# Kernel tuning notes

Measured on AMD Instinct MI355X. Metric: run time of the kernel, lower is better.

## Reference

```python
import math
from itertools import product
import jax, jax.numpy as jnp
import numpy as np

# ---- static config (mirrors LPD.__init__) ----
IMG_W, IMG_H = 1920, 1080
MIN_SIZES = [[10, 16, 24], [32, 48], [64, 96], [128, 192, 256]]
STEPS = [8, 16, 32, 64]
VARIANCE = (0.1, 0.2)
CONF_THR = 0.3
NMS_THR = 0.3
TOP_K = 2000
KEEP_TOP_K = 750
BATCH = 16


def make_priors() -> np.ndarray:
    """Anchor grid in normalized (cx, cy, w, h), kornia _PriorBox order:
    per level, per cell (row-major), per min_size."""
    levels = []
    for step, mss in zip(STEPS, MIN_SIZES):
        fh, fw = math.ceil(IMG_H / step), math.ceil(IMG_W / step)
        ii, jj = np.meshgrid(np.arange(fh), np.arange(fw), indexing='ij')
        cx = (jj + 0.5) * step / IMG_W  # [fh, fw]
        cy = (ii + 0.5) * step / IMG_H
        nms_ = len(mss)
        cx = np.broadcast_to(cx[..., None], (fh, fw, nms_))
        cy = np.broadcast_to(cy[..., None], (fh, fw, nms_))
        skx = np.broadcast_to(np.array(mss, np.float64) / IMG_W, (fh, fw, nms_))
        sky = np.broadcast_to(np.array(mss, np.float64) / IMG_H, (fh, fw, nms_))
        levels.append(np.stack([cx, cy, skx, sky], -1).reshape(-1, 4))
    return np.concatenate(levels, 0).astype(np.float32)  # [N, 4]

N_PRIORS = make_priors().shape[0]  # 119130 for 1920x1080


def decode(loc, priors):
    """loc [B,N,14], priors [N,4] -> scaled [B,N,14] (x1y1x2y2 + 5 landmarks)."""
    var = jnp.asarray(VARIANCE, loc.dtype)
    p_xy, p_wh = priors[:, :2], priors[:, 2:4]
    cxcy = p_xy + loc[..., 0:2] * VARIANCE[0] * p_wh
    wh = p_wh * jnp.exp(loc[..., 2:4] * var)
    x1y1 = cxcy - wh * 0.5
    x2y2 = x1y1 + wh
    # 5 landmark points
    lmk = p_xy[None, :, None, :] + loc[..., 4:14].reshape(*loc.shape[:-1], 5, 2) * VARIANCE[0] * p_wh[None, :, None, :]
    boxes = jnp.concatenate([x1y1, x2y2, lmk.reshape(*loc.shape[:-1], 10)], -1)
    scale = jnp.tile(jnp.asarray([IMG_W, IMG_H], loc.dtype), 7)
    return boxes * scale


def nms_keep(b, s):
    """Greedy NMS. b [K,4] sorted by descending score s [K]. Returns bool keep [K]."""
    area = jnp.clip(b[:, 2] - b[:, 0], 0.0) * jnp.clip(b[:, 3] - b[:, 1], 0.0)
    lt = jnp.maximum(b[:, None, :2], b[None, :, :2])
    rb = jnp.minimum(b[:, None, 2:4], b[None, :, 2:4])
    whi = jnp.clip(rb - lt, 0.0)
    inter = whi[..., 0] * whi[..., 1]
    iou_m = inter / (area[:, None] + area[None, :] - inter + 1e-9)  # [K,K]
    K = b.shape[0]
    idx = jnp.arange(K)

    def step(active, i):
        keep_i = active[i]
        active = active & ~(keep_i & (iou_m[i] > NMS_THR) & (idx > i))
        return active, keep_i

    _, keep = jax.lax.scan(step, s > 0.0, idx)
    return keep


def setup_inputs() -> dict:
    key = jax.random.key(0)
    k1, k2, k3 = jax.random.split(key, 3)
    return {
        'loc': jax.random.normal(k1, (BATCH, N_PRIORS, 14), jnp.float32),
        'conf': jax.random.normal(k2, (BATCH, N_PRIORS, 2), jnp.float32),
        'iou': jax.random.normal(k3, (BATCH, N_PRIORS, 1), jnp.float32),
    }


def reference(loc, conf, iou):
    priors = jnp.asarray(make_priors())  # [N,4] constant
    cls = jax.nn.softmax(conf, axis=-1)[..., 1]          # [B,N]
    iou_s = jnp.clip(iou[..., 0], 0.0, 1.0)
    scores = jnp.sqrt(cls * iou_s)
    scores = jnp.where(scores >= CONF_THR, scores, 0.0)  # confidence threshold
    boxes = decode(loc, priors)                          # [B,N,14]
    top_s, top_i = jax.lax.top_k(scores, TOP_K)          # sorted desc
    boxes_k = jnp.take_along_axis(boxes, top_i[..., None], axis=1)  # [B,K,14]
    keep = jax.vmap(nms_keep)(boxes_k[..., :4], top_s)   # [B,K] bool
    keep = keep & (jnp.cumsum(keep.astype(jnp.int32), axis=-1) <= KEEP_TOP_K)
    dets = jnp.concatenate([boxes_k, (top_s * keep)[..., None]], -1)  # [B,K,15]
    return dets
```

## Files before the change

### kernel.cpp

```cpp
#include <hip/hip_runtime.h>
#include <math.h>

#define BB 16
#define TOPK 2000
#define KEEPK 750
#define CAND_CAP 4096
#define EDGE_CAP 8192
#define HIST_BINS 256
#define BIN_BASE 0x3E99u

__global__ __launch_bounds__(256) void k_scores(const float* __restrict__ conf,
                                                const float* __restrict__ iou,
                                                unsigned* __restrict__ sbits,
                                                unsigned* __restrict__ hist,
                                                unsigned* __restrict__ ccount,
                                                unsigned* __restrict__ ecount,
                                                unsigned* __restrict__ tdone,
                                                int N, int nchunk) {
  __shared__ unsigned h[HIST_BINS];
  int b = blockIdx.y;
  int tid = threadIdx.x;
  for (int i = tid; i < HIST_BINS; i += 256) h[i] = 0;
  if (blockIdx.x == 0) {
    if (tid == 0) ccount[b] = 0;
    if (tid == 1) ecount[b] = 0;
    if (tid == 2) tdone[b] = 0;
  }
  __syncthreads();
  const float2* c2 = (const float2*)conf + (size_t)b * N;
  const float* iu = iou + (size_t)b * N;
  unsigned* sb = sbits + (size_t)b * N;
  int n0 = blockIdx.x * 4096;
#pragma unroll 4
  for (int k = 0; k < 16; ++k) {
    int n = n0 + k * 256 + tid;
    if (n < N) {
      float2 c = c2[n];
      float m = fmaxf(c.x, c.y);
      float e0 = (float)exp((double)(c.x - m));
      float e1 = (float)exp((double)(c.y - m));
      float p1 = e1 / (e0 + e1);
      float ic = fminf(fmaxf(iu[n], 0.0f), 1.0f);
      float s = sqrtf(p1 * ic);
      s = (s >= 0.3f) ? s : 0.0f;
      unsigned bits = __float_as_uint(s);
      sb[n] = bits;
      if (bits != 0u) {
        int bin = (int)(bits >> 16) - (int)BIN_BASE;
        bin = bin < 0 ? 0 : (bin > 255 ? 255 : bin);
        atomicAdd(&h[bin], 1u);
      }
    }
  }
  __syncthreads();
  unsigned* hdst = hist + ((size_t)b * nchunk + blockIdx.x) * HIST_BINS;
  for (int i = tid; i < HIST_BINS; i += 256) hdst[i] = h[i];
}

__global__ __launch_bounds__(256) void k_compact(const unsigned* __restrict__ sbits,
                                                 const unsigned* __restrict__ hist,
                                                 unsigned* __restrict__ ccount,
                                                 unsigned long long* __restrict__ ckeys,
                                                 int N, int nchunk) {
  __shared__ unsigned sT;
  __shared__ unsigned long long masks[32];
  __shared__ unsigned wioff[32];
  __shared__ unsigned blockbase;
  int b = blockIdx.y;
  int tid = threadIdx.x, lane = tid & 63, wv = tid >> 6;

  if (tid < 64) {
    const unsigned* h = hist + (size_t)b * nchunk * HIST_BINS;
    unsigned v0 = 0, v1 = 0, v2 = 0, v3 = 0;
    int b0 = 255 - (4 * lane + 0), b1 = 255 - (4 * lane + 1);
    int b2 = 255 - (4 * lane + 2), b3 = 255 - (4 * lane + 3);
    for (int c = 0; c < nchunk; ++c) {
      const unsigned* hc = h + c * HIST_BINS;
      v0 += hc[b0]; v1 += hc[b1]; v2 += hc[b2]; v3 += hc[b3];
    }
    unsigned p0 = v0, p1 = p0 + v1, p2 = p1 + v2, p3 = p2 + v3;
    unsigned tot = p3, pre = tot;
    for (int off = 1; off < 64; off <<= 1) {
      unsigned q = __shfl_up(pre, off);
      if (lane >= off) pre += q;
    }
    unsigned excl = pre - tot;
    int kk = -1;
    if (excl + p0 >= TOPK) kk = 0;
    else if (excl + p1 >= TOPK) kk = 1;
    else if (excl + p2 >= TOPK) kk = 2;
    else if (excl + p3 >= TOPK) kk = 3;
    unsigned long long m = __ballot(kk >= 0);
    int bin = 0;
    if (m != 0ull) {
      int fl = __ffsll((unsigned long long)m) - 1;
      int fk = __shfl(kk, fl);
      bin = 255 - (4 * fl + fk);
    }
    if (lane == 0) sT = ((unsigned)(BIN_BASE + (unsigned)bin)) << 16;
  }
  __syncthreads();
  unsigned T = sT;

  const unsigned* sb = sbits + (size_t)b * N;
  int n0 = blockIdx.x * 2048;
  unsigned v[8];
  unsigned long long mk[8];
#pragma unroll
  for (int k = 0; k < 8; ++k) {
    int n = n0 + k * 256 + tid;
    v[k] = (n < N) ? sb[n] : 0u;
    bool p = v[k] >= T;
    mk[k] = __ballot(p);
    if (lane == 0) masks[k * 4 + wv] = mk[k];
  }
  __syncthreads();
  if (tid < 64) {
    unsigned c = (tid < 32) ? (unsigned)__popcll(masks[tid]) : 0u;
    unsigned pre = c;
    for (int off = 1; off < 64; off <<= 1) {
      unsigned q = __shfl_up(pre, off);
      if (lane >= off) pre += q;
    }
    if (tid < 32) wioff[tid] = pre - c;
    if (tid == 31) blockbase = atomicAdd(&ccount[b], pre);
  }
  __syncthreads();
  unsigned base = blockbase;
#pragma unroll
  for (int k = 0; k < 8; ++k) {
    if ((mk[k] >> lane) & 1ull) {
      unsigned pos = base + wioff[k * 4 + wv] +
                     (unsigned)__popcll(mk[k] & ((1ull << lane) - 1ull));
      if (pos < CAND_CAP) {
        int n = n0 + k * 256 + tid;
        ckeys[(size_t)b * CAND_CAP + pos] =
            ((unsigned long long)v[k] << 32) | (unsigned)(~(unsigned)n);
      }
    }
  }
}

__global__ __launch_bounds__(256) void k_sort1(const unsigned* __restrict__ ccount,
                                               unsigned long long* __restrict__ ckeys) {
  __shared__ unsigned long long s[1024];
  int b = blockIdx.x >> 2, chunk = blockIdx.x & 3;
  bool asc = (chunk & 1) != 0;
  int t = threadIdx.x;
  unsigned c = ccount[b];
  if (c > CAND_CAP) c = CAND_CAP;
  unsigned long long* base = ckeys + (size_t)b * CAND_CAP + chunk * 1024;
  int goff = chunk * 1024;
  unsigned long long key[4];
#pragma unroll
  for (int e = 0; e < 4; ++e) {
    int g = goff + 4 * t + e;
    key[e] = (g < (int)c) ? base[4 * t + e] : 0ull;
  }
  for (int k = 2; k <= 1024; k <<= 1) {
    for (int j = k >> 1; j > 0; j >>= 1) {
      if (j >= 256) {
        __syncthreads();
#pragma unroll
        for (int e = 0; e < 4; ++e) s[4 * t + e] = key[e];
        __syncthreads();
        int pbase = (4 * t) ^ j;
        bool own_lo = ((4 * t) & j) == 0;
        bool dir = (((4 * t) & k) == 0) != asc;
        bool keep_max = (own_lo == dir);
#pragma unroll
        for (int e = 0; e < 4; ++e) {
          unsigned long long o = s[pbase + e];
          unsigned long long mx = key[e] > o ? key[e] : o;
          unsigned long long mn = key[e] > o ? o : key[e];
          key[e] = keep_max ? mx : mn;
        }
      } else if (j >= 4) {
        int d = j >> 2;
        bool own_lo = (t & d) == 0;
        bool dir = (((4 * t) & k) == 0) != asc;
        bool keep_max = (own_lo == dir);
#pragma unroll
        for (int e = 0; e < 4; ++e) {
          unsigned long long o = __shfl_xor(key[e], d, 64);
          unsigned long long mx = key[e] > o ? key[e] : o;
          unsigned long long mn = key[e] > o ? o : key[e];
          key[e] = keep_max ? mx : mn;
        }
      } else {
#pragma unroll
        for (int e = 0; e < 4; ++e) {
          int p = e ^ j;
          if (p > e) {
            int i = 4 * t + e;
            bool dir = (((i & k) == 0) != asc);
            bool need = dir ? (key[e] < key[p]) : (key[e] > key[p]);
            if (need) { unsigned long long tmp = key[e]; key[e] = key[p]; key[p] = tmp; }
          }
        }
      }
    }
  }
#pragma unroll
  for (int e = 0; e < 4; ++e) base[4 * t + e] = key[e];
}

__global__ __launch_bounds__(1024) void k_sort2_decode(
    const unsigned long long* __restrict__ ckeys, const float* __restrict__ loc,
    float* __restrict__ top_s, float* __restrict__ out,
    float4* __restrict__ boxes4, int N) {
  __shared__ unsigned long long s[CAND_CAP];
  int b = blockIdx.x;
  int t = threadIdx.x;
  const unsigned long long* src = ckeys + (size_t)b * CAND_CAP;
  unsigned long long key[4];
#pragma unroll
  for (int e = 0; e < 4; ++e) key[e] = src[4 * t + e];
  for (int k = 2048; k <= CAND_CAP; k <<= 1) {
    for (int j = k >> 1; j > 0; j >>= 1) {
      if (j >= 256) {
        __syncthreads();
#pragma unroll
        for (int e = 0; e < 4; ++e) s[4 * t + e] = key[e];
        __syncthreads();
        int pbase = (4 * t) ^ j;
        bool own_lo = ((4 * t) & j) == 0;
        bool dir = ((4 * t) & k) == 0;
        bool keep_max = (own_lo == dir);
#pragma unroll
        for (int e = 0; e < 4; ++e) {
          unsigned long long o = s[pbase + e];
          unsigned long long mx = key[e] > o ? key[e] : o;
          unsigned long long mn = key[e] > o ? o : key[e];
          key[e] = keep_max ? mx : mn;
        }
      } else if (j >= 4) {
        int d = j >> 2;
        bool own_lo = (t & d) == 0;
        bool dir = ((4 * t) & k) == 0;
        bool keep_max = (own_lo == dir);
#pragma unroll
        for (int e = 0; e < 4; ++e) {
          unsigned long long o = __shfl_xor(key[e], d, 64);
          unsigned long long mx = key[e] > o ? key[e] : o;
          unsigned long long mn = key[e] > o ? o : key[e];
          key[e] = keep_max ? mx : mn;
        }
      } else {
#pragma unroll
        for (int e = 0; e < 4; ++e) {
          int p = e ^ j;
          if (p > e) {
            int i = 4 * t + e;
            bool dir = ((i & k) == 0);
            bool need = dir ? (key[e] < key[p]) : (key[e] > key[p]);
            if (need) { unsigned long long tmp = key[e]; key[e] = key[p]; key[p] = tmp; }
          }
        }
      }
    }
  }
  if (t < TOPK / 4) {
#pragma unroll
    for (int e = 0; e < 4; ++e) {
      int r = 4 * t + e;
      unsigned long long kk = key[e];
      float sv = __uint_as_float((unsigned)(kk >> 32));
      top_s[b * TOPK + r] = sv;
      unsigned idxu = ~(unsigned)kk;
      if (idxu >= (unsigned)N) idxu = 0;
      int i = (int)idxu;
      int off, fw, st, nm, lvl;
      if (i < 97200)       { lvl = 0; off = 0;      fw = 240; st = 8;  nm = 3; }
      else if (i < 113520) { lvl = 1; off = 97200;  fw = 120; st = 16; nm = 2; }
      else if (i < 117600) { lvl = 2; off = 113520; fw = 60;  st = 32; nm = 2; }
      else                 { lvl = 3; off = 117600; fw = 30;  st = 64; nm = 3; }
      int tt = i - off;
      int cell = tt / nm;
      int kms = tt - cell * nm;
      int row = cell / fw;
      int col = cell - row * fw;
      int msv = (lvl == 0) ? (kms == 0 ? 10 : (kms == 1 ? 16 : 24))
              : (lvl == 1) ? (kms == 0 ? 32 : 48)
              : (lvl == 2) ? (kms == 0 ? 64 : 96)
                           : (kms == 0 ? 128 : (kms == 1 ? 192 : 256));
      float cx  = (float)(((double)col + 0.5) * (double)st / 1920.0);
      float cy  = (float)(((double)row + 0.5) * (double)st / 1080.0);
      float skx = (float)((double)msv / 1920.0);
      float sky = (float)((double)msv / 1080.0);
      const float2* lp2 = (const float2*)(loc + ((size_t)b * N + (size_t)i) * 14);
      float l[14];
#pragma unroll
      for (int q = 0; q < 7; ++q) { float2 v = lp2[q]; l[2 * q] = v.x; l[2 * q + 1] = v.y; }
      float cx2 = cx + (l[0] * 0.1f) * skx;
      float cy2 = cy + (l[1] * 0.1f) * sky;
      float wx = skx * expf(l[2] * 0.1f);
      float wy = sky * expf(l[3] * 0.2f);
      float x1 = cx2 - wx * 0.5f, y1 = cy2 - wy * 0.5f;
      float x2 = x1 + wx, y2 = y1 + wy;
      float X1 = x1 * 1920.0f, Y1 = y1 * 1080.0f, X2 = x2 * 1920.0f, Y2 = y2 * 1080.0f;
      float* o = out + ((size_t)b * TOPK + r) * 15;
      o[0] = X1; o[1] = Y1; o[2] = X2; o[3] = Y2;
#pragma unroll
      for (int q = 0; q < 5; ++q) {
        o[4 + 2 * q] = (cx + (l[4 + 2 * q] * 0.1f) * skx) * 1920.0f;
        o[5 + 2 * q] = (cy + (l[5 + 2 * q] * 0.1f) * sky) * 1080.0f;
      }
      boxes4[b * TOPK + r] = make_float4(X1, Y1, X2, Y2);
    }
  }
}

__global__ __launch_bounds__(256) void k_edges_nms(const float4* __restrict__ boxes4,
                                                   const float* __restrict__ top_s,
                                                   unsigned* __restrict__ ecount,
                                                   unsigned* __restrict__ edges,
                                                   unsigned* __restrict__ tdone,
                                                   float* __restrict__ out) {
  __shared__ float4 cb[256];
  __shared__ unsigned loc_e[1024];
  __shared__ unsigned lcnt, gbase;
  __shared__ int is_last;
  int b = blockIdx.y;
  int t = blockIdx.x;
  int ib = 0;
  while ((ib + 1) * (ib + 2) / 2 <= t) ++ib;
  int jb = t - ib * (ib + 1) / 2;
  int tid = threadIdx.x;
  if (tid == 0) lcnt = 0;
  int j0 = jb * 256;
  {
    int j = j0 + tid;
    cb[tid] = (j < TOPK) ? boxes4[b * TOPK + j]
                         : make_float4(-1e30f, -1e30f, -1e30f, -1e30f);
  }
  __syncthreads();
  int r = ib * 256 + tid;
  bool valid = r < TOPK;
  float4 A4 = valid ? boxes4[b * TOPK + r] : make_float4(0, 0, 0, 0);
  float areaA = fmaxf(A4.z - A4.x, 0.f) * fmaxf(A4.w - A4.y, 0.f);
  int cmax = r - j0;
  if (cmax > 256) cmax = 256;
  if (!valid) cmax = 0;
  for (int c = 0; c < cmax; ++c) {
    float4 Bx = cb[c];
    float xx1 = fmaxf(A4.x, Bx.x), yy1 = fmaxf(A4.y, Bx.y);
    float xx2 = fminf(A4.z, Bx.z), yy2 = fminf(A4.w, Bx.w);
    float w = fmaxf(xx2 - xx1, 0.f), hgt = fmaxf(yy2 - yy1, 0.f);
    float inter = w * hgt;
    float areaB = fmaxf(Bx.z - Bx.x, 0.f) * fmaxf(Bx.w - Bx.y, 0.f);
    float iouv = inter / (areaA + areaB - inter + 1e-9f);
    if (iouv > 0.3f) {
      unsigned p = atomicAdd(&lcnt, 1u);
      if (p < 1024u) loc_e[p] = ((unsigned)r << 16) | (unsigned)(j0 + c);
    }
  }
  __syncthreads();
  unsigned cnt = lcnt;
  if (cnt > 1024u) cnt = 1024u;
  if (tid == 0 && cnt) gbase = atomicAdd(&ecount[b], cnt);
  __syncthreads();
  if (cnt)
    for (unsigned e = tid; e < cnt; e += 256) {
      unsigned p = gbase + e;
      if (p < EDGE_CAP) edges[b * EDGE_CAP + p] = loc_e[e];
    }
  __syncthreads();
  __threadfence();
  if (tid == 0) {
    unsigned done = atomicAdd(&tdone[b], 1u);
    is_last = (done == 35u);
  }
  __syncthreads();
  if (!is_last) return;
  __threadfence();

  __shared__ unsigned long long Am[32], K[32], S[32];
  __shared__ unsigned pref[32];
  __shared__ unsigned ecache[2048];
  __shared__ int changed;
  int lane = tid & 63, wv = tid >> 6;
  for (int base = 0; base < 2048; base += 256) {
    int i = base + tid;
    bool act = (i < TOPK) && (top_s[b * TOPK + i] > 0.0f);
    unsigned long long m = __ballot(act);
    if (lane == 0) { int w = (base >> 6) + wv; Am[w] = m; K[w] = m; }
  }
  unsigned E = ecount[b];
  if (E > EDGE_CAP) E = EDGE_CAP;
  unsigned Ec = E > 2048u ? 2048u : E;
  for (unsigned e = tid; e < Ec; e += 256) ecache[e] = edges[b * EDGE_CAP + e];
  __syncthreads();
  for (int it = 0; it < 32; ++it) {
    if (tid == 0) changed = 0;
    if (tid < 32) S[tid] = 0ull;
    __syncthreads();
    for (unsigned e = tid; e < Ec; e += 256) {
      unsigned v = ecache[e];
      unsigned i = v >> 16, j = v & 0xFFFFu;
      if ((K[j >> 6] >> (j & 63)) & 1ull) atomicOr(&S[i >> 6], 1ull << (i & 63));
    }
    for (unsigned e = 2048u + tid; e < E; e += 256) {
      unsigned v = edges[b * EDGE_CAP + e];
      unsigned i = v >> 16, j = v & 0xFFFFu;
      if ((K[j >> 6] >> (j & 63)) & 1ull) atomicOr(&S[i >> 6], 1ull << (i & 63));
    }
    __syncthreads();
    if (tid < 32) {
      unsigned long long nk = Am[tid] & ~S[tid];
      if (nk != K[tid]) { K[tid] = nk; changed = 1; }
    }
    __syncthreads();
    if (!changed) break;
  }
  if (tid == 0) {
    unsigned acc = 0;
    for (int w = 0; w < 32; ++w) { pref[w] = acc; acc += (unsigned)__popcll(K[w]); }
  }
  __syncthreads();
  for (int base = 0; base < 2048; base += 256) {
    int i = base + tid;
    if (i < TOPK) {
      int w = i >> 6;
      unsigned long long bit = (K[w] >> (i & 63)) & 1ull;
      unsigned rank = pref[w] + (unsigned)__popcll(K[w] & ((1ull << (i & 63)) - 1ull)) +
                      (unsigned)bit;
      float sv = top_s[b * TOPK + i];
      out[((size_t)b * TOPK + i) * 15 + 14] = (bit && rank <= KEEPK) ? sv : 0.0f;
    }
  }
}

extern "C" void kernel_launch(void* const* d_in, const int* in_sizes, int n_in,
                              void* d_out, int out_size, void* d_ws, size_t ws_size,
                              hipStream_t stream) {
  const float* loc  = (const float*)d_in[0];
  const float* conf = (const float*)d_in[1];
  const float* iou  = (const float*)d_in[2];
  float* out = (float*)d_out;
  int N = in_sizes[2] / BB;
  int nchunk = (N + 4095) / 4096;

  char* ws = (char*)d_ws;
  size_t off = 0;
  unsigned* ccount = (unsigned*)(ws + off); off += 64;
  unsigned* ecount = (unsigned*)(ws + off); off += 64;
  unsigned* tdone  = (unsigned*)(ws + off); off += 64;
  off = (off + 255) & ~(size_t)255;
  unsigned* hist   = (unsigned*)(ws + off); off += (size_t)BB * nchunk * HIST_BINS * 4;
  unsigned* sbits  = (unsigned*)(ws + off); off += (size_t)BB * N * 4;
  off = (off + 15) & ~(size_t)15;
  unsigned long long* ckeys = (unsigned long long*)(ws + off); off += (size_t)BB * CAND_CAP * 8;
  float* top_s = (float*)(ws + off);       off += (size_t)BB * TOPK * 4;
  off = (off + 15) & ~(size_t)15;
  float4* boxes4 = (float4*)(ws + off);    off += (size_t)BB * TOPK * 16;
  unsigned* edges = (unsigned*)(ws + off); off += (size_t)BB * EDGE_CAP * 4;

  k_scores<<<dim3(nchunk, BB), 256, 0, stream>>>(conf, iou, sbits, hist,
                                                 ccount, ecount, tdone, N, nchunk);
  k_compact<<<dim3((N + 2047) / 2048, BB), 256, 0, stream>>>(sbits, hist, ccount,
                                                             ckeys, N, nchunk);
  k_sort1<<<BB * 4, 256, 0, stream>>>(ccount, ckeys);
  k_sort2_decode<<<BB, 1024, 0, stream>>>(ckeys, loc, top_s, out, boxes4, N);
  k_edges_nms<<<dim3(36, BB), 256, 0, stream>>>(boxes4, top_s, ecount, edges, tdone, out);
}
```

Measured before the change: 312.0 us.

## Replace iterative fixed-point NMS with chunked exact greedy NMS over bucketed edges

The fused edge+NMS kernel is split into two kernels. The edge kernel now uses 128-thread tiles with SoA shared boxes and a division-free IoU test, and writes suppression edges into per-64-row buckets. The NMS kernel walks the 64-box chunks in order, applying cross-chunk suppression from already-kept boxes and resolving in-chunk greedy order serially on one thread. This removes the last-block atomic handoff and the repeated full-edge fixed-point iterations, at the cost of an extra launch and a serial single-thread inner loop per chunk.

```diff
diff --git a/kernel.cpp b/kernel.cpp
--- a/kernel.cpp
+++ b/kernel.cpp
@@ -5,26 +5,25 @@
 #define TOPK 2000
 #define KEEPK 750
 #define CAND_CAP 4096
-#define EDGE_CAP 8192
 #define HIST_BINS 256
 #define BIN_BASE 0x3E99u
+#define NBUCK 32
+#define BUCK_CAP 512
 
 __global__ __launch_bounds__(256) void k_scores(const float* __restrict__ conf,
                                                 const float* __restrict__ iou,
                                                 unsigned* __restrict__ sbits,
                                                 unsigned* __restrict__ hist,
                                                 unsigned* __restrict__ ccount,
-                                                unsigned* __restrict__ ecount,
-                                                unsigned* __restrict__ tdone,
+                                                unsigned* __restrict__ ebc,
                                                 int N, int nchunk) {
   __shared__ unsigned h[HIST_BINS];
   int b = blockIdx.y;
   int tid = threadIdx.x;
   for (int i = tid; i < HIST_BINS; i += 256) h[i] = 0;
   if (blockIdx.x == 0) {
-    if (tid == 0) ccount[b] = 0;
-    if (tid == 1) ecount[b] = 0;
-    if (tid == 2) tdone[b] = 0;
+    if (tid < NBUCK) ebc[b * NBUCK + tid] = 0;
+    if (tid == NBUCK) ccount[b] = 0;
   }
   __syncthreads();
   const float2* c2 = (const float2*)conf + (size_t)b * N;
@@ -311,107 +310,123 @@
   }
 }
 
-__global__ __launch_bounds__(256) void k_edges_nms(const float4* __restrict__ boxes4,
-                                                   const float* __restrict__ top_s,
-                                                   unsigned* __restrict__ ecount,
-                                                   unsigned* __restrict__ edges,
-                                                   unsigned* __restrict__ tdone,
-                                                   float* __restrict__ out) {
-  __shared__ float4 cb[256];
-  __shared__ unsigned loc_e[1024];
-  __shared__ unsigned lcnt, gbase;
-  __shared__ int is_last;
+__global__ __launch_bounds__(128) void k_edges(const float4* __restrict__ boxes4,
+                                               unsigned* __restrict__ ebc,
+                                               unsigned* __restrict__ ebuck) {
+  __shared__ float bx1[128], by1[128], bx2[128], by2[128], bta[128];
+  __shared__ unsigned l0[1024], l1[1024];
+  __shared__ unsigned c0, c1, base0, base1;
   int b = blockIdx.y;
   int t = blockIdx.x;
-  int ib = 0;
-  while ((ib + 1) * (ib + 2) / 2 <= t) ++ib;
-  int jb = t - ib * (ib + 1) / 2;
+  int it = 0;
+  while ((it + 1) * (it + 2) / 2 <= t) ++it;
+  int jt = t - it * (it + 1) / 2;
   int tid = threadIdx.x;
-  if (tid == 0) lcnt = 0;
-  int j0 = jb * 256;
+  if (tid == 0) { c0 = 0; c1 = 0; }
+  int j0 = jt * 128;
   {
     int j = j0 + tid;
-    cb[tid] = (j < TOPK) ? boxes4[b * TOPK + j]
-                         : make_float4(-1e30f, -1e30f, -1e30f, -1e30f);
-  }
-  __syncthreads();
-  int r = ib * 256 + tid;
-  bool valid = r < TOPK;
-  float4 A4 = valid ? boxes4[b * TOPK + r] : make_float4(0, 0, 0, 0);
-  float areaA = fmaxf(A4.z - A4.x, 0.f) * fmaxf(A4.w - A4.y, 0.f);
-  int cmax = r - j0;
-  if (cmax > 256) cmax = 256;
-  if (!valid) cmax = 0;
-  for (int c = 0; c < cmax; ++c) {
-    float4 Bx = cb[c];
-    float xx1 = fmaxf(A4.x, Bx.x), yy1 = fmaxf(A4.y, Bx.y);
-    float xx2 = fminf(A4.z, Bx.z), yy2 = fminf(A4.w, Bx.w);
-    float w = fmaxf(xx2 - xx1, 0.f), hgt = fmaxf(yy2 - yy1, 0.f);
-    float inter = w * hgt;
-    float areaB = fmaxf(Bx.z - Bx.x, 0.f) * fmaxf(Bx.w - Bx.y, 0.f);
-    float iouv = inter / (areaA + areaB - inter + 1e-9f);
-    if (iouv > 0.3f) {
-      unsigned p = atomicAdd(&lcnt, 1u);
-      if (p < 1024u) loc_e[p] = ((unsigned)r << 16) | (unsigned)(j0 + c);
-    }
-  }
-  __syncthreads();
-  unsigned cnt = lcnt;
-  if (cnt > 1024u) cnt = 1024u;
-  if (tid == 0 && cnt) gbase = atomicAdd(&ecount[b], cnt);
-  __syncthreads();
-  if (cnt)
-    for (unsigned e = tid; e < cnt; e += 256) {
-      unsigned p = gbase + e;
-      if (p < EDGE_CAP) edges[b * EDGE_CAP + p] = loc_e[e];
-    }
-  __syncthreads();
-  __threadfence();
-  if (tid == 0) {
-    unsigned done = atomicAdd(&tdone[b], 1u);
-    is_last = (done == 35u);
-  }
-  __syncthreads();
-  if (!is_last) return;
-  __threadfence();
-
-  __shared__ unsigned long long Am[32], K[32], S[32];
+    if (j < TOPK) {
+      float4 Bj = boxes4[b * TOPK + j];
+      bx1[tid] = Bj.x; by1[tid] = Bj.y; bx2[tid] = Bj.z; by2[tid] = Bj.w;
+      bta[tid] = 0.3f * (fmaxf(Bj.z - Bj.x, 0.f) * fmaxf(Bj.w - Bj.y, 0.f));
+    } else {
+      bx1[tid] = 1e30f; by1[tid] = 1e30f; bx2[tid] = -1e30f; by2[tid] = -1e30f;
+      bta[tid] = 0.f;
+    }
+  }
+  __syncthreads();
+  int i = it * 128 + tid;
+  int jmax = 0;
+  float4 A4 = make_float4(0, 0, 0, 0);
+  float taA = 0.f;
+  if (i < TOPK) {
+    A4 = boxes4[b * TOPK + i];
+    taA = 0.3f * (fmaxf(A4.z - A4.x, 0.f) * fmaxf(A4.w - A4.y, 0.f));
+    jmax = i - j0; if (jmax > 128) jmax = 128;
+  }
+  bool hibuck = tid >= 64;
+  for (int c = 0; c < jmax; ++c) {
+    float xx1 = fmaxf(A4.x, bx1[c]), yy1 = fmaxf(A4.y, by1[c]);
+    float xx2 = fminf(A4.z, bx2[c]), yy2 = fminf(A4.w, by2[c]);
+    float w = fmaxf(xx2 - xx1, 0.f), h = fmaxf(yy2 - yy1, 0.f);
+    float inter = w * h;
+    if (inter * 1.3f > taA + bta[c] + 3e-10f) {
+      unsigned enc = ((unsigned)i << 16) | (unsigned)(j0 + c);
+      if (!hibuck) { unsigned p = atomicAdd(&c0, 1u); if (p < 1024u) l0[p] = enc; }
+      else         { unsigned p = atomicAdd(&c1, 1u); if (p < 1024u) l1[p] = enc; }
+    }
+  }
+  __syncthreads();
+  unsigned n0 = c0 > 1024u ? 1024u : c0, n1 = c1 > 1024u ? 1024u : c1;
+  if (tid == 0 && n0) base0 = atomicAdd(&ebc[b * NBUCK + 2 * it], n0);
+  if (tid == 1 && n1) base1 = atomicAdd(&ebc[b * NBUCK + 2 * it + 1], n1);
+  __syncthreads();
+  unsigned* d0 = ebuck + ((size_t)b * NBUCK + 2 * it) * BUCK_CAP;
+  unsigned* d1 = ebuck + ((size_t)b * NBUCK + 2 * it + 1) * BUCK_CAP;
+  for (unsigned e = tid; e < n0; e += 128) {
+    unsigned p = base0 + e; if (p < BUCK_CAP) d0[p] = l0[e];
+  }
+  for (unsigned e = tid; e < n1; e += 128) {
+    unsigned p = base1 + e; if (p < BUCK_CAP) d1[p] = l1[e];
+  }
+}
+
+__global__ __launch_bounds__(256) void k_nms(const float* __restrict__ top_s,
+                                             const unsigned* __restrict__ ebc,
+                                             const unsigned* __restrict__ ebuck,
+                                             float* __restrict__ out) {
+  int b = blockIdx.x;
+  __shared__ unsigned long long A[32], K[32];
+  __shared__ unsigned sup[2];
+  __shared__ unsigned ilist[256];
+  __shared__ unsigned icnt;
   __shared__ unsigned pref[32];
-  __shared__ unsigned ecache[2048];
-  __shared__ int changed;
-  int lane = tid & 63, wv = tid >> 6;
+  int tid = threadIdx.x, lane = tid & 63, wv = tid >> 6;
   for (int base = 0; base < 2048; base += 256) {
     int i = base + tid;
     bool act = (i < TOPK) && (top_s[b * TOPK + i] > 0.0f);
     unsigned long long m = __ballot(act);
-    if (lane == 0) { int w = (base >> 6) + wv; Am[w] = m; K[w] = m; }
-  }
-  unsigned E = ecount[b];
-  if (E > EDGE_CAP) E = EDGE_CAP;
-  unsigned Ec = E > 2048u ? 2048u : E;
-  for (unsigned e = tid; e < Ec; e += 256) ecache[e] = edges[b * EDGE_CAP + e];
-  __syncthreads();
-  for (int it = 0; it < 32; ++it) {
-    if (tid == 0) changed = 0;
-    if (tid < 32) S[tid] = 0ull;
+    if (lane == 0) { int w = (base >> 6) + wv; A[w] = m; K[w] = 0ull; }
+  }
+  __syncthreads();
+  for (int c = 0; c < 32; ++c) {
+    if (tid == 0) { sup[0] = 0u; sup[1] = 0u; icnt = 0u; }
     __syncthreads();
-    for (unsigned e = tid; e < Ec; e += 256) {
-      unsigned v = ecache[e];
+    unsigned cnt = ebc[b * NBUCK + c];
+    if (cnt > BUCK_CAP) cnt = BUCK_CAP;
+    const unsigned* src = ebuck + ((size_t)b * NBUCK + c) * BUCK_CAP;
+    for (unsigned e = tid; e < cnt; e += 256) {
+      unsigned v = src[e];
       unsigned i = v >> 16, j = v & 0xFFFFu;
-      if ((K[j >> 6] >> (j & 63)) & 1ull) atomicOr(&S[i >> 6], 1ull << (i & 63));
-    }
-    for (unsigned e = 2048u + tid; e < E; e += 256) {
-      unsigned v = edges[b * EDGE_CAP + e];
-      unsigned i = v >> 16, j = v & 0xFFFFu;
-      if ((K[j >> 6] >> (j & 63)) & 1ull) atomicOr(&S[i >> 6], 1ull << (i & 63));
+      int jc = (int)(j >> 6);
+      if (jc < c) {
+        if ((K[jc] >> (j & 63)) & 1ull)
+          atomicOr(&sup[(i >> 5) & 1], 1u << (i & 31));
+      } else {
+        unsigned p = atomicAdd(&icnt, 1u);
+        if (p < 256u) ilist[p] = v;
+      }
     }
     __syncthreads();
-    if (tid < 32) {
-      unsigned long long nk = Am[tid] & ~S[tid];
-      if (nk != K[tid]) { K[tid] = nk; changed = 1; }
+    if (tid == 0) {
+      unsigned long long supw = ((unsigned long long)sup[1] << 32) | (unsigned long long)sup[0];
+      unsigned long long cand = A[c] & ~supw;
+      unsigned long long kept = 0ull;
+      unsigned m = icnt > 256u ? 256u : icnt;
+      while (cand) {
+        int l = __ffsll(cand) - 1;
+        kept |= 1ull << l;
+        cand &= ~(1ull << l);
+        unsigned jfull = (unsigned)(c * 64 + l);
+        for (unsigned e = 0; e < m; ++e) {
+          unsigned v = ilist[e];
+          if ((v & 0xFFFFu) == jfull) cand &= ~(1ull << ((v >> 16) & 63));
+        }
+      }
+      K[c] = kept;
     }
     __syncthreads();
-    if (!changed) break;
   }
   if (tid == 0) {
     unsigned acc = 0;
@@ -444,8 +459,7 @@
   char* ws = (char*)d_ws;
   size_t off = 0;
   unsigned* ccount = (unsigned*)(ws + off); off += 64;
-  unsigned* ecount = (unsigned*)(ws + off); off += 64;
-  unsigned* tdone  = (unsigned*)(ws + off); off += 64;
+  unsigned* ebc    = (unsigned*)(ws + off); off += (size_t)BB * NBUCK * 4;
   off = (off + 255) & ~(size_t)255;
   unsigned* hist   = (unsigned*)(ws + off); off += (size_t)BB * nchunk * HIST_BINS * 4;
   unsigned* sbits  = (unsigned*)(ws + off); off += (size_t)BB * N * 4;
@@ -454,13 +468,14 @@
   float* top_s = (float*)(ws + off);       off += (size_t)BB * TOPK * 4;
   off = (off + 15) & ~(size_t)15;
   float4* boxes4 = (float4*)(ws + off);    off += (size_t)BB * TOPK * 16;
-  unsigned* edges = (unsigned*)(ws + off); off += (size_t)BB * EDGE_CAP * 4;
-
-  k_scores<<<dim3(nchunk, BB), 256, 0, stream>>>(conf, iou, sbits, hist,
-                                                 ccount, ecount, tdone, N, nchunk);
+  unsigned* ebuck = (unsigned*)(ws + off); off += (size_t)BB * NBUCK * BUCK_CAP * 4;
+
+  k_scores<<<dim3(nchunk, BB), 256, 0, stream>>>(conf, iou, sbits, hist, ccount, ebc,
+                                                 N, nchunk);
   k_compact<<<dim3((N + 2047) / 2048, BB), 256, 0, stream>>>(sbits, hist, ccount,
                                                              ckeys, N, nchunk);
   k_sort1<<<BB * 4, 256, 0, stream>>>(ccount, ckeys);
   k_sort2_decode<<<BB, 1024, 0, stream>>>(ckeys, loc, top_s, out, boxes4, N);
-  k_edges_nms<<<dim3(36, BB), 256, 0, stream>>>(boxes4, top_s, ecount, edges, tdone, out);
-}
+  k_edges<<<dim3(136, BB), 128, 0, stream>>>(boxes4, ebc, ebuck);
+  k_nms<<<BB, 256, 0, stream>>>(top_s, ebc, ebuck, out);
+}
```

Result: slower. 366.8 us (+17.6%).

## Split fused edge+NMS kernel, use 128-wide triangle tiles and division-free IoU test

Applied to the files above, without the earlier changes.

Splits the last-block-finishes pattern into a separate edge-building kernel and a per-batch NMS kernel, which removes the done counter and threadfences. Edge tiles shrink from 256 to 128 wide (136 blocks per batch instead of 36) to spread the triangular pairwise IoU work across more CUs. Boxes are stored structure-of-arrays in shared memory, and the IoU division is replaced by a multiply-compare against precomputed 0.3*area terms. The NMS kernel's shared edge cache grows to 4096 entries. The costs are an extra kernel launch and slightly different rounding near the threshold.

```diff
diff --git a/kernel.cpp b/kernel.cpp
--- a/kernel.cpp
+++ b/kernel.cpp
@@ -15,7 +15,6 @@
                                                 unsigned* __restrict__ hist,
                                                 unsigned* __restrict__ ccount,
                                                 unsigned* __restrict__ ecount,
-                                                unsigned* __restrict__ tdone,
                                                 int N, int nchunk) {
   __shared__ unsigned h[HIST_BINS];
   int b = blockIdx.y;
@@ -24,7 +23,6 @@
   if (blockIdx.x == 0) {
     if (tid == 0) ccount[b] = 0;
     if (tid == 1) ecount[b] = 0;
-    if (tid == 2) tdone[b] = 0;
   }
   __syncthreads();
   const float2* c2 = (const float2*)conf + (size_t)b * N;
@@ -311,85 +309,84 @@
   }
 }
 
-__global__ __launch_bounds__(256) void k_edges_nms(const float4* __restrict__ boxes4,
-                                                   const float* __restrict__ top_s,
-                                                   unsigned* __restrict__ ecount,
-                                                   unsigned* __restrict__ edges,
-                                                   unsigned* __restrict__ tdone,
-                                                   float* __restrict__ out) {
-  __shared__ float4 cb[256];
+__global__ __launch_bounds__(128) void k_edges(const float4* __restrict__ boxes4,
+                                               unsigned* __restrict__ ecount,
+                                               unsigned* __restrict__ edges) {
+  __shared__ float bx1[128], by1[128], bx2[128], by2[128], bta[128];
   __shared__ unsigned loc_e[1024];
   __shared__ unsigned lcnt, gbase;
-  __shared__ int is_last;
   int b = blockIdx.y;
   int t = blockIdx.x;
-  int ib = 0;
-  while ((ib + 1) * (ib + 2) / 2 <= t) ++ib;
-  int jb = t - ib * (ib + 1) / 2;
+  int it = 0;
+  while ((it + 1) * (it + 2) / 2 <= t) ++it;
+  int jt = t - it * (it + 1) / 2;
   int tid = threadIdx.x;
   if (tid == 0) lcnt = 0;
-  int j0 = jb * 256;
+  int j0 = jt * 128;
   {
     int j = j0 + tid;
-    cb[tid] = (j < TOPK) ? boxes4[b * TOPK + j]
-                         : make_float4(-1e30f, -1e30f, -1e30f, -1e30f);
-  }
-  __syncthreads();
-  int r = ib * 256 + tid;
-  bool valid = r < TOPK;
-  float4 A4 = valid ? boxes4[b * TOPK + r] : make_float4(0, 0, 0, 0);
-  float areaA = fmaxf(A4.z - A4.x, 0.f) * fmaxf(A4.w - A4.y, 0.f);
-  int cmax = r - j0;
-  if (cmax > 256) cmax = 256;
-  if (!valid) cmax = 0;
-  for (int c = 0; c < cmax; ++c) {
-    float4 Bx = cb[c];
-    float xx1 = fmaxf(A4.x, Bx.x), yy1 = fmaxf(A4.y, Bx.y);
-    float xx2 = fminf(A4.z, Bx.z), yy2 = fminf(A4.w, Bx.w);
-    float w = fmaxf(xx2 - xx1, 0.f), hgt = fmaxf(yy2 - yy1, 0.f);
-    float inter = w * hgt;
-    float areaB = fmaxf(Bx.z - Bx.x, 0.f) * fmaxf(Bx.w - Bx.y, 0.f);
-    float iouv = inter / (areaA + areaB - inter + 1e-9f);
-    if (iouv > 0.3f) {
+    if (j < TOPK) {
+      float4 Bj = boxes4[b * TOPK + j];
+      bx1[tid] = Bj.x; by1[tid] = Bj.y; bx2[tid] = Bj.z; by2[tid] = Bj.w;
+      bta[tid] = 0.3f * (fmaxf(Bj.z - Bj.x, 0.f) * fmaxf(Bj.w - Bj.y, 0.f));
+    } else {
+      bx1[tid] = 1e30f; by1[tid] = 1e30f; bx2[tid] = -1e30f; by2[tid] = -1e30f;
+      bta[tid] = 0.f;
+    }
+  }
+  __syncthreads();
+  int i = it * 128 + tid;
+  int jmax = 0;
+  float4 A4 = make_float4(0, 0, 0, 0);
+  float taA = 0.f;
+  if (i < TOPK) {
+    A4 = boxes4[b * TOPK + i];
+    taA = 0.3f * (fmaxf(A4.z - A4.x, 0.f) * fmaxf(A4.w - A4.y, 0.f));
+    jmax = i - j0; if (jmax > 128) jmax = 128;
+  }
+  for (int c = 0; c < jmax; ++c) {
+    float xx1 = fmaxf(A4.x, bx1[c]), yy1 = fmaxf(A4.y, by1[c]);
+    float xx2 = fminf(A4.z, bx2[c]), yy2 = fminf(A4.w, by2[c]);
+    float w = fmaxf(xx2 - xx1, 0.f), h = fmaxf(yy2 - yy1, 0.f);
+    float inter = w * h;
+    if (inter * 1.3f > taA + bta[c] + 3e-10f) {
       unsigned p = atomicAdd(&lcnt, 1u);
-      if (p < 1024u) loc_e[p] = ((unsigned)r << 16) | (unsigned)(j0 + c);
-    }
-  }
-  __syncthreads();
-  unsigned cnt = lcnt;
-  if (cnt > 1024u) cnt = 1024u;
+      if (p < 1024u) loc_e[p] = ((unsigned)i << 16) | (unsigned)(j0 + c);
+    }
+  }
+  __syncthreads();
+  unsigned cnt = lcnt > 1024u ? 1024u : lcnt;
   if (tid == 0 && cnt) gbase = atomicAdd(&ecount[b], cnt);
   __syncthreads();
-  if (cnt)
-    for (unsigned e = tid; e < cnt; e += 256) {
+  if (cnt) {
+    unsigned* dst = edges + (size_t)b * EDGE_CAP;
+    for (unsigned e = tid; e < cnt; e += 128) {
       unsigned p = gbase + e;
-      if (p < EDGE_CAP) edges[b * EDGE_CAP + p] = loc_e[e];
-    }
-  __syncthreads();
-  __threadfence();
-  if (tid == 0) {
-    unsigned done = atomicAdd(&tdone[b], 1u);
-    is_last = (done == 35u);
-  }
-  __syncthreads();
-  if (!is_last) return;
-  __threadfence();
-
-  __shared__ unsigned long long Am[32], K[32], S[32];
+      if (p < EDGE_CAP) dst[p] = loc_e[e];
+    }
+  }
+}
+
+__global__ __launch_bounds__(256) void k_nms(const float* __restrict__ top_s,
+                                             const unsigned* __restrict__ ecount,
+                                             const unsigned* __restrict__ edges,
+                                             float* __restrict__ out) {
+  int b = blockIdx.x;
+  __shared__ unsigned long long A[32], K[32], S[32];
   __shared__ unsigned pref[32];
-  __shared__ unsigned ecache[2048];
+  __shared__ unsigned ecache[4096];
   __shared__ int changed;
-  int lane = tid & 63, wv = tid >> 6;
+  int tid = threadIdx.x, lane = tid & 63, wv = tid >> 6;
   for (int base = 0; base < 2048; base += 256) {
     int i = base + tid;
     bool act = (i < TOPK) && (top_s[b * TOPK + i] > 0.0f);
     unsigned long long m = __ballot(act);
-    if (lane == 0) { int w = (base >> 6) + wv; Am[w] = m; K[w] = m; }
+    if (lane == 0) { int w = (base >> 6) + wv; A[w] = m; K[w] = m; }
   }
   unsigned E = ecount[b];
   if (E > EDGE_CAP) E = EDGE_CAP;
-  unsigned Ec = E > 2048u ? 2048u : E;
-  for (unsigned e = tid; e < Ec; e += 256) ecache[e] = edges[b * EDGE_CAP + e];
+  unsigned Ec = E > 4096u ? 4096u : E;
+  for (unsigned e = tid; e < Ec; e += 256) ecache[e] = edges[(size_t)b * EDGE_CAP + e];
   __syncthreads();
   for (int it = 0; it < 32; ++it) {
     if (tid == 0) changed = 0;
@@ -400,14 +397,14 @@
       unsigned i = v >> 16, j = v & 0xFFFFu;
       if ((K[j >> 6] >> (j & 63)) & 1ull) atomicOr(&S[i >> 6], 1ull << (i & 63));
     }
-    for (unsigned e = 2048u + tid; e < E; e += 256) {
-      unsigned v = edges[b * EDGE_CAP + e];
+    for (unsigned e = 4096u + tid; e < E; e += 256) {
+      unsigned v = edges[(size_t)b * EDGE_CAP + e];
       unsigned i = v >> 16, j = v & 0xFFFFu;
       if ((K[j >> 6] >> (j & 63)) & 1ull) atomicOr(&S[i >> 6], 1ull << (i & 63));
     }
     __syncthreads();
     if (tid < 32) {
-      unsigned long long nk = Am[tid] & ~S[tid];
+      unsigned long long nk = A[tid] & ~S[tid];
       if (nk != K[tid]) { K[tid] = nk; changed = 1; }
     }
     __syncthreads();
@@ -445,7 +442,6 @@
   size_t off = 0;
   unsigned* ccount = (unsigned*)(ws + off); off += 64;
   unsigned* ecount = (unsigned*)(ws + off); off += 64;
-  unsigned* tdone  = (unsigned*)(ws + off); off += 64;
   off = (off + 255) & ~(size_t)255;
   unsigned* hist   = (unsigned*)(ws + off); off += (size_t)BB * nchunk * HIST_BINS * 4;
   unsigned* sbits  = (unsigned*)(ws + off); off += (size_t)BB * N * 4;
@@ -456,11 +452,12 @@
   float4* boxes4 = (float4*)(ws + off);    off += (size_t)BB * TOPK * 16;
   unsigned* edges = (unsigned*)(ws + off); off += (size_t)BB * EDGE_CAP * 4;
 
-  k_scores<<<dim3(nchunk, BB), 256, 0, stream>>>(conf, iou, sbits, hist,
-                                                 ccount, ecount, tdone, N, nchunk);
+  k_scores<<<dim3(nchunk, BB), 256, 0, stream>>>(conf, iou, sbits, hist, ccount,
+                                                 ecount, N, nchunk);
   k_compact<<<dim3((N + 2047) / 2048, BB), 256, 0, stream>>>(sbits, hist, ccount,
                                                              ckeys, N, nchunk);
   k_sort1<<<BB * 4, 256, 0, stream>>>(ccount, ckeys);
   k_sort2_decode<<<BB, 1024, 0, stream>>>(ckeys, loc, top_s, out, boxes4, N);
-  k_edges_nms<<<dim3(36, BB), 256, 0, stream>>>(boxes4, top_s, ecount, edges, tdone, out);
-}
+  k_edges<<<dim3(136, BB), 128, 0, stream>>>(boxes4, ecount, edges);
+  k_nms<<<BB, 256, 0, stream>>>(top_s, ecount, edges, out);
+}
```

New measurement: 270.2 us. 1.15x faster.
